# Optimization experiments

Measured on AMD Instinct MI355X. Metric: run time of the kernel, lower is better.

The kernel has to match this reference:

```python
import jax, jax.numpy as jnp
import numpy as np
import math

NUM_HEADS = 16
LOGIT_SCALE_MAX = math.log(1.0 / 0.01)  # log(100)
EPS = 1e-12


def _l2norm(x):
    # F.normalize(x, dim=-1): x / max(||x||_2, eps)
    n = jnp.sqrt(jnp.sum(x * x, axis=-1, keepdims=True))
    return x / jnp.maximum(n, EPS)


def setup_inputs() -> dict:
    key = jax.random.key(0)
    ks = jax.random.split(key, 6)
    N, B, C = 1024, 4, 1024
    scale = (C // NUM_HEADS) ** -0.5
    return {
        "query": jax.random.normal(ks[0], (N, B, C), jnp.float32),
        "key": jax.random.normal(ks[1], (N, B, C), jnp.float32),
        "value": jax.random.normal(ks[2], (N, B, C), jnp.float32),
        "in_proj_w": jax.random.normal(ks[3], (3 * C, C), jnp.float32) * scale,
        "in_proj_b": jnp.zeros((3 * C,), jnp.float32),
        "logit_scale": jnp.log(10.0) * jnp.ones((NUM_HEADS, 1, 1), jnp.float32),
        "out_w": jax.random.normal(ks[4], (C, C), jnp.float32) * scale,
        "out_b": jnp.zeros((C,), jnp.float32),
    }


def reference(query, key, value, in_proj_w, in_proj_b, logit_scale, out_w, out_b):
    N, B, C = query.shape
    H = NUM_HEADS
    hd = C // H
    # packed in-projection, split into q/k/v pieces
    w_q, w_k, w_v = jnp.split(in_proj_w, 3, axis=0)
    b_q, b_k, b_v = jnp.split(in_proj_b, 3, axis=0)
    q = query @ w_q.T + b_q          # (N, B, C)
    k = key @ w_k.T + b_k
    v = value @ w_v.T + b_v
    # (N, B, C) -> (B*H, N, hd)
    q = q.reshape(N, B * H, hd).swapaxes(0, 1)
    k = k.reshape(N, B * H, hd).swapaxes(0, 1)
    v = v.reshape(N, B * H, hd).swapaxes(0, 1)
    # cosine-similarity scores with learnable per-head logit scale
    attn = jnp.einsum('bqd,bkd->bqk', _l2norm(q), _l2norm(k))  # (B*H, N, N)
    ls = jnp.exp(jnp.minimum(logit_scale, LOGIT_SCALE_MAX))     # (H,1,1)
    attn = (attn.reshape(B, H, N, N) * ls).reshape(B * H, N, N)
    attn = jax.nn.softmax(attn, axis=-1)
    x = jnp.einsum('bqk,bkd->bqd', attn, v)                     # (B*H, N, hd)
    x = x.swapaxes(0, 1).reshape(N, B, C)
    return x @ out_w.T + out_b
```

## Files before the change

### kernel.cpp

```cpp
#include <hip/hip_runtime.h>


typedef _Float16 f16x8 __attribute__((ext_vector_type(8)));
typedef __fp16   h16x2 __attribute__((ext_vector_type(2)));
typedef float    f32x4 __attribute__((ext_vector_type(4)));

#define LOG2E 1.4426950408889634f
#define LOGMAX 4.6051702f

#define GLOAD16(g, l) \
    __builtin_amdgcn_global_load_lds((__attribute__((address_space(1))) void*)(g), \
                                     (__attribute__((address_space(3))) void*)(l), 16, 0, 0)

__device__ __forceinline__ unsigned short f2h(float x) {
    union { _Float16 h; unsigned short u; } cv;
    cv.h = (_Float16)x;
    return cv.u;
}

__global__ __launch_bounds__(256) void cvt_all(
    const float* __restrict__ q, const float* __restrict__ k,
    const float* __restrict__ v, const float* __restrict__ w,
    const float* __restrict__ ow,
    unsigned short* __restrict__ qbf, unsigned short* __restrict__ kbf,
    unsigned short* __restrict__ vbf, unsigned short* __restrict__ wbf,
    unsigned short* __restrict__ owbf)
{
    int b = blockIdx.x;
    const float* src; unsigned short* dst; int idx;
    if      (b < 4096)  { src = q;  dst = qbf;  idx = b; }
    else if (b < 8192)  { src = k;  dst = kbf;  idx = b - 4096; }
    else if (b < 12288) { src = v;  dst = vbf;  idx = b - 8192; }
    else if (b < 15360) { src = w;  dst = wbf;  idx = b - 12288; }
    else                { src = ow; dst = owbf; idx = b - 15360; }
    int i = idx * 256 + threadIdx.x;
    float4 val = ((const float4*)src)[i];
    ushort4 o;
    o.x = f2h(val.x); o.y = f2h(val.y); o.z = f2h(val.z); o.w = f2h(val.w);
    ((ushort4*)dst)[i] = o;
}

__global__ __launch_bounds__(256) void proj_gemm(
    const unsigned short* __restrict__ qbf, const unsigned short* __restrict__ kbf,
    const unsigned short* __restrict__ vbf, const unsigned short* __restrict__ wbf,
    const float* __restrict__ bias, const float* __restrict__ lsc,
    unsigned short* __restrict__ qn, unsigned short* __restrict__ kn,
    unsigned short* __restrict__ vT)
{
    __shared__ __align__(16) unsigned short AsmF[128 * 64];
    __shared__ __align__(16) unsigned short BsmF[128 * 64];
    int tid = threadIdx.x;
    int lane = tid & 63, wave = tid >> 6;
    int lr = lane & 15, lq = lane >> 4;
    int wr = wave >> 1, wc = wave & 1;

    int lin = blockIdx.x;
    int xcd = lin & 7, s = lin >> 3;
    int xt = s & 7, yy = (s >> 3) & 3, z = s >> 5;
    int m0 = (xcd * 4 + yy) * 128, n0 = xt * 128;

    const unsigned short* A = (z == 0) ? qbf : (z == 1) ? kbf : vbf;
    const unsigned short* W = wbf + (size_t)z * 1024 * 1024;

    int rl = lane >> 3;
    int cg = ((lane & 7) ^ rl) << 3;
    const unsigned short* gA = A + (size_t)(m0 + wave * 32 + rl) * 1024 + cg;
    const unsigned short* gB = W + (size_t)(n0 + wave * 32 + rl) * 1024 + cg;
    unsigned short* lA = &AsmF[wave * 32 * 64];
    unsigned short* lB = &BsmF[wave * 32 * 64];

    int swz = lr & 7;
    int c0 = (lq ^ swz) << 3;
    int c1 = ((lq ^ 4) ^ swz) << 3;

    f32x4 acc[4][4];
    for (int i = 0; i < 4; i++) for (int j = 0; j < 4; j++) acc[i][j] = (f32x4){0.f, 0.f, 0.f, 0.f};

    for (int ki = 0; ki < 16; ++ki) {
        for (int j = 0; j < 4; ++j) {
            GLOAD16(gA + ki * 64 + j * 8192, lA + j * 512);
            GLOAD16(gB + ki * 64 + j * 8192, lB + j * 512);
        }
        __syncthreads();
        for (int kc = 0; kc < 2; ++kc) {
            int co = kc ? c1 : c0;
            f16x8 af[4], bfr[4];
            for (int mi = 0; mi < 4; ++mi) af[mi]  = *(const f16x8*)&AsmF[(wr * 64 + mi * 16 + lr) * 64 + co];
            for (int ni = 0; ni < 4; ++ni) bfr[ni] = *(const f16x8*)&BsmF[(wc * 64 + ni * 16 + lr) * 64 + co];
            for (int mi = 0; mi < 4; ++mi)
                for (int ni = 0; ni < 4; ++ni)
                    acc[mi][ni] = __builtin_amdgcn_mfma_f32_16x16x32_f16(af[mi], bfr[ni], acc[mi][ni], 0, 0, 0);
        }
        __syncthreads();
    }

    int h = (n0 >> 6) + wc;
    float bv[4];
    for (int ni = 0; ni < 4; ++ni) bv[ni] = bias[z * 1024 + n0 + wc * 64 + ni * 16 + lr];
    for (int mi = 0; mi < 4; ++mi)
        for (int ni = 0; ni < 4; ++ni)
            for (int r = 0; r < 4; ++r) acc[mi][ni][r] += bv[ni];

    float lsfac = __expf(fminf(lsc[h], LOGMAX)) * LOG2E;

    for (int mi = 0; mi < 4; ++mi)
        for (int r = 0; r < 4; ++r) {
            int row = m0 + wr * 64 + mi * 16 + lq * 4 + r;
            int n = row >> 2, b = row & 3;
            int bh = b * 16 + h;
            if (z < 2) {
                float ss = 0.f;
                for (int ni = 0; ni < 4; ++ni) ss += acc[mi][ni][r] * acc[mi][ni][r];
                for (int off = 1; off < 16; off <<= 1) ss += __shfl_xor(ss, off);
                float scale = 1.0f / fmaxf(sqrtf(ss), 1e-12f);
                if (z == 0) scale *= lsfac;
                unsigned short* dst = (z == 0) ? qn : kn;
                for (int ni = 0; ni < 4; ++ni)
                    dst[(size_t)bh * 65536 + (size_t)n * 64 + ni * 16 + lr] = f2h(acc[mi][ni][r] * scale);
            } else {
                for (int ni = 0; ni < 4; ++ni)
                    vT[(size_t)bh * 65536 + (size_t)(ni * 16 + lr) * 1024 + n] = f2h(acc[mi][ni][r]);
            }
        }
}

__global__ __launch_bounds__(256) void flash_kernel(
    const unsigned short* __restrict__ qn, const unsigned short* __restrict__ kn,
    const unsigned short* __restrict__ vT, const float* __restrict__ lsc,
    unsigned short* __restrict__ xb)
{
    __shared__ __align__(16) unsigned short K_flat[2][64 * 64];
    __shared__ __align__(16) unsigned short V_flat[2][64 * 64];
    __shared__ __align__(16) unsigned short P_lds[4][2][16][72];
    int tid = threadIdx.x;
    int lane = tid & 63, wave = tid >> 6;
    int lr = lane & 15, lq = lane >> 4;

    int lin = blockIdx.x;
    int xcd = lin & 7, s = lin >> 3;
    int qt = s & 7, bh = xcd * 8 + (s >> 3);
    int q0 = qt * 128;

    float off = __expf(fminf(lsc[bh & 15], LOGMAX)) * LOG2E - 12.0f;
    f32x4 initv = (f32x4){-off, -off, -off, -off};

    f16x8 qf[2][2];
    for (int g = 0; g < 2; ++g)
        for (int kc = 0; kc < 2; ++kc)
            qf[g][kc] = *(const f16x8*)(qn + (size_t)bh * 65536 +
                          (size_t)(q0 + g * 64 + wave * 16 + lr) * 64 + kc * 32 + lq * 8);

    int rl = lane >> 3;
    int cg = ((lane & 7) ^ rl) << 3;
    const unsigned short* gK = kn + (size_t)bh * 65536 + (size_t)(wave * 16 + rl) * 64 + cg;
    const unsigned short* gV = vT + (size_t)bh * 65536 + (size_t)(wave * 16 + rl) * 1024 + cg;
    int swz = lr & 7;
    int c0 = (lq ^ swz) << 3;
    int c1 = ((lq ^ 4) ^ swz) << 3;

    f32x4 o[2][4];
    for (int g = 0; g < 2; ++g) for (int i = 0; i < 4; i++) o[g][i] = (f32x4){0.f, 0.f, 0.f, 0.f};
    float lsum[2] = {0.f, 0.f};

    {
        unsigned short* lK = &K_flat[0][wave * 16 * 64];
        unsigned short* lV = &V_flat[0][wave * 16 * 64];
        for (int j = 0; j < 2; ++j) {
            GLOAD16(gK + j * 512,  lK + j * 512);
            GLOAD16(gV + j * 8192, lV + j * 512);
        }
    }

    for (int kt = 0; kt < 16; ++kt) {
        int cur = kt & 1;
        __syncthreads();

        if (kt < 15) {
            unsigned short* lK = &K_flat[cur ^ 1][wave * 16 * 64];
            unsigned short* lV = &V_flat[cur ^ 1][wave * 16 * 64];
            for (int j = 0; j < 2; ++j) {
                GLOAD16(gK + (kt + 1) * 4096 + j * 512,  lK + j * 512);
                GLOAD16(gV + (kt + 1) * 64  + j * 8192,  lV + j * 512);
            }
        }

        f32x4 sc[2][4];
        __builtin_amdgcn_s_setprio(1);
        for (int ct = 0; ct < 4; ++ct) {
            for (int kc = 0; kc < 2; ++kc) {
                f16x8 kf = *(const f16x8*)&K_flat[cur][(ct * 16 + lr) * 64 + (kc ? c1 : c0)];
                for (int g = 0; g < 2; ++g)
                    sc[g][ct] = __builtin_amdgcn_mfma_f32_16x16x32_f16(
                        kf, qf[g][kc], kc == 0 ? initv : sc[g][ct], 0, 0, 0);
            }
        }
        __builtin_amdgcn_s_setprio(0);

        for (int g = 0; g < 2; ++g)
            for (int ct = 0; ct < 4; ++ct) {
                float p0 = __builtin_amdgcn_exp2f(sc[g][ct][0]);
                float p1 = __builtin_amdgcn_exp2f(sc[g][ct][1]);
                float p2 = __builtin_amdgcn_exp2f(sc[g][ct][2]);
                float p3 = __builtin_amdgcn_exp2f(sc[g][ct][3]);
                lsum[g] += (p0 + p1) + (p2 + p3);
                union { h16x2 h[2]; ushort4 u; } pw;
                pw.h[0] = __builtin_amdgcn_cvt_pkrtz(p0, p1);
                pw.h[1] = __builtin_amdgcn_cvt_pkrtz(p2, p3);
                *(ushort4*)&P_lds[wave][g][lr][ct * 16 + lq * 4] = pw.u;
            }

        f16x8 pf[2][2];
        for (int g = 0; g < 2; ++g)
            for (int kc = 0; kc < 2; ++kc)
                pf[g][kc] = *(const f16x8*)&P_lds[wave][g][lr][kc * 32 + lq * 8];
        __builtin_amdgcn_s_setprio(1);
        for (int nt = 0; nt < 4; ++nt)
            for (int kc = 0; kc < 2; ++kc) {
                f16x8 vf = *(const f16x8*)&V_flat[cur][(nt * 16 + lr) * 64 + (kc ? c1 : c0)];
                for (int g = 0; g < 2; ++g)
                    o[g][nt] = __builtin_amdgcn_mfma_f32_16x16x32_f16(vf, pf[g][kc], o[g][nt], 0, 0, 0);
            }
        __builtin_amdgcn_s_setprio(0);
    }

    int b = bh >> 4, h = bh & 15;
    for (int g = 0; g < 2; ++g) {
        float ls = lsum[g];
        ls += __shfl_xor(ls, 16);
        ls += __shfl_xor(ls, 32);
        float inv = 1.0f / ls;
        size_t m = (size_t)(q0 + g * 64 + wave * 16 + lr) * 4 + b;
        for (int nt = 0; nt < 4; ++nt) {
            ushort4 w;
            w.x = f2h(o[g][nt][0] * inv); w.y = f2h(o[g][nt][1] * inv);
            w.z = f2h(o[g][nt][2] * inv); w.w = f2h(o[g][nt][3] * inv);
            *(ushort4*)(xb + m * 1024 + h * 64 + nt * 16 + lq * 4) = w;
        }
    }
}

__global__ __launch_bounds__(256) void out_gemm(
    const unsigned short* __restrict__ xb, const unsigned short* __restrict__ owbf,
    const float* __restrict__ bias, float* __restrict__ outp)
{
    __shared__ __align__(16) unsigned short AsmF[128 * 64];
    __shared__ __align__(16) unsigned short BsmF[64 * 64];
    int tid = threadIdx.x;
    int lane = tid & 63, wave = tid >> 6;
    int lr = lane & 15, lq = lane >> 4;

    int lin = blockIdx.x;
    int xcd = lin & 7, s = lin >> 3;
    int xt = s & 15, yy = s >> 4;
    int m0 = (xcd * 4 + yy) * 128, n0 = xt * 64;

    int rl = lane >> 3;
    int cg = ((lane & 7) ^ rl) << 3;
    const unsigned short* gA = xb   + (size_t)(m0 + wave * 32 + rl) * 1024 + cg;
    const unsigned short* gB = owbf + (size_t)(n0 + wave * 16 + rl) * 1024 + cg;
    unsigned short* lA = &AsmF[wave * 32 * 64];
    unsigned short* lB = &BsmF[wave * 16 * 64];
    int swz = lr & 7;
    int c0 = (lq ^ swz) << 3;
    int c1 = ((lq ^ 4) ^ swz) << 3;

    f32x4 acc[2][4];
    for (int i = 0; i < 2; i++) for (int j = 0; j < 4; j++) acc[i][j] = (f32x4){0.f, 0.f, 0.f, 0.f};

    for (int ki = 0; ki < 16; ++ki) {
        for (int j = 0; j < 4; ++j)
            GLOAD16(gA + ki * 64 + j * 8192, lA + j * 512);
        for (int j = 0; j < 2; ++j)
            GLOAD16(gB + ki * 64 + j * 8192, lB + j * 512);
        __syncthreads();
        for (int kc = 0; kc < 2; ++kc) {
            int co = kc ? c1 : c0;
            f16x8 af[2], bfr[4];
            for (int mi = 0; mi < 2; ++mi) af[mi]  = *(const f16x8*)&AsmF[(wave * 32 + mi * 16 + lr) * 64 + co];
            for (int ni = 0; ni < 4; ++ni) bfr[ni] = *(const f16x8*)&BsmF[(ni * 16 + lr) * 64 + co];
            for (int mi = 0; mi < 2; ++mi)
                for (int ni = 0; ni < 4; ++ni)
                    acc[mi][ni] = __builtin_amdgcn_mfma_f32_16x16x32_f16(af[mi], bfr[ni], acc[mi][ni], 0, 0, 0);
        }
        __syncthreads();
    }
    for (int mi = 0; mi < 2; ++mi)
        for (int ni = 0; ni < 4; ++ni)
            for (int r = 0; r < 4; ++r) {
                int row = m0 + wave * 32 + mi * 16 + lq * 4 + r;
                int col = n0 + ni * 16 + lr;
                outp[(size_t)row * 1024 + col] = acc[mi][ni][r] + bias[col];
            }
}

extern "C" void kernel_launch(void* const* d_in, const int* in_sizes, int n_in,
                              void* d_out, int out_size, void* d_ws, size_t ws_size,
                              hipStream_t stream) {
    const float* query = (const float*)d_in[0];
    const float* key   = (const float*)d_in[1];
    const float* value = (const float*)d_in[2];
    const float* ipw   = (const float*)d_in[3];
    const float* ipb   = (const float*)d_in[4];
    const float* lsc   = (const float*)d_in[5];
    const float* ow    = (const float*)d_in[6];
    const float* ob    = (const float*)d_in[7];
    float* outp = (float*)d_out;

    char* ws = (char*)d_ws;
    unsigned short* qbf  = (unsigned short*)(ws);
    unsigned short* kbf  = (unsigned short*)(ws + 8388608);
    unsigned short* vbf  = (unsigned short*)(ws + 16777216);
    unsigned short* wbf  = (unsigned short*)(ws + 25165824);
    unsigned short* owbf = (unsigned short*)(ws + 31457280);
    unsigned short* qn   = (unsigned short*)(ws + 33554432);
    unsigned short* kn   = (unsigned short*)(ws + 41943040);
    unsigned short* vT   = (unsigned short*)(ws + 50331648);
    unsigned short* xbuf = (unsigned short*)(ws + 58720256);

    cvt_all<<<16384, 256, 0, stream>>>(query, key, value, ipw, ow,
                                       qbf, kbf, vbf, wbf, owbf);
    proj_gemm<<<768, 256, 0, stream>>>(qbf, kbf, vbf, wbf, ipb, lsc, qn, kn, vT);
    flash_kernel<<<512, 256, 0, stream>>>(qn, kn, vT, lsc, xbuf);
    out_gemm<<<512, 256, 0, stream>>>(xbuf, owbf, ob, outp);
}
```

Measured before the change: 203.8 us.

## Fuse fp32-to-fp16 conversion into GEMM loads with double-buffered LDS pipeline

Removes the separate conversion kernel and its fp16 workspace copies. proj_gemm and out_gemm now load fp32 inputs and weights into registers, convert them to fp16, and store them into double-buffered LDS, prefetching the next k-slice while MFMAs run. The goal is to avoid a full extra read/write pass over the activations and weights. In exchange the GEMMs read twice as many bytes per tile, use a smaller k-step of 32, and rely on register staging instead of direct global-to-LDS loads for the converted operands.

```diff
diff --git a/kernel.cpp b/kernel.cpp
--- a/kernel.cpp
+++ b/kernel.cpp
@@ -18,37 +18,22 @@
     return cv.u;
 }
 
-__global__ __launch_bounds__(256) void cvt_all(
-    const float* __restrict__ q, const float* __restrict__ k,
-    const float* __restrict__ v, const float* __restrict__ w,
-    const float* __restrict__ ow,
-    unsigned short* __restrict__ qbf, unsigned short* __restrict__ kbf,
-    unsigned short* __restrict__ vbf, unsigned short* __restrict__ wbf,
-    unsigned short* __restrict__ owbf)
-{
-    int b = blockIdx.x;
-    const float* src; unsigned short* dst; int idx;
-    if      (b < 4096)  { src = q;  dst = qbf;  idx = b; }
-    else if (b < 8192)  { src = k;  dst = kbf;  idx = b - 4096; }
-    else if (b < 12288) { src = v;  dst = vbf;  idx = b - 8192; }
-    else if (b < 15360) { src = w;  dst = wbf;  idx = b - 12288; }
-    else                { src = ow; dst = owbf; idx = b - 15360; }
-    int i = idx * 256 + threadIdx.x;
-    float4 val = ((const float4*)src)[i];
-    ushort4 o;
-    o.x = f2h(val.x); o.y = f2h(val.y); o.z = f2h(val.z); o.w = f2h(val.w);
-    ((ushort4*)dst)[i] = o;
+__device__ __forceinline__ f16x8 cvt8(float4 a, float4 b) {
+    f16x8 v;
+    v[0] = (_Float16)a.x; v[1] = (_Float16)a.y; v[2] = (_Float16)a.z; v[3] = (_Float16)a.w;
+    v[4] = (_Float16)b.x; v[5] = (_Float16)b.y; v[6] = (_Float16)b.z; v[7] = (_Float16)b.w;
+    return v;
 }
 
 __global__ __launch_bounds__(256) void proj_gemm(
-    const unsigned short* __restrict__ qbf, const unsigned short* __restrict__ kbf,
-    const unsigned short* __restrict__ vbf, const unsigned short* __restrict__ wbf,
+    const float* __restrict__ qsrc, const float* __restrict__ ksrc,
+    const float* __restrict__ vsrc, const float* __restrict__ wsrc,
     const float* __restrict__ bias, const float* __restrict__ lsc,
     unsigned short* __restrict__ qn, unsigned short* __restrict__ kn,
     unsigned short* __restrict__ vT)
 {
-    __shared__ __align__(16) unsigned short AsmF[128 * 64];
-    __shared__ __align__(16) unsigned short BsmF[128 * 64];
+    __shared__ __align__(16) unsigned short Asm[2][4096];
+    __shared__ __align__(16) unsigned short Bsm[2][4096];
     int tid = threadIdx.x;
     int lane = tid & 63, wave = tid >> 6;
     int lr = lane & 15, lq = lane >> 4;
@@ -59,39 +44,58 @@
     int xt = s & 7, yy = (s >> 3) & 3, z = s >> 5;
     int m0 = (xcd * 4 + yy) * 128, n0 = xt * 128;
 
-    const unsigned short* A = (z == 0) ? qbf : (z == 1) ? kbf : vbf;
-    const unsigned short* W = wbf + (size_t)z * 1024 * 1024;
-
-    int rl = lane >> 3;
-    int cg = ((lane & 7) ^ rl) << 3;
-    const unsigned short* gA = A + (size_t)(m0 + wave * 32 + rl) * 1024 + cg;
-    const unsigned short* gB = W + (size_t)(n0 + wave * 32 + rl) * 1024 + cg;
-    unsigned short* lA = &AsmF[wave * 32 * 64];
-    unsigned short* lB = &BsmF[wave * 32 * 64];
-
-    int swz = lr & 7;
-    int c0 = (lq ^ swz) << 3;
-    int c1 = ((lq ^ 4) ^ swz) << 3;
+    const float* A = (z == 0) ? qsrc : (z == 1) ? ksrc : vsrc;
+    const float* W = wsrc + (size_t)z * 1048576;
+
+    int r4 = lane >> 2, c4 = lane & 3;
+    int ssw = (r4 >> 1) & 3;
+    const float* gA = A + (size_t)(m0 + wave * 32 + r4) * 1024 + c4 * 8;
+    const float* gB = W + (size_t)(n0 + wave * 32 + r4) * 1024 + c4 * 8;
+    int wo = (wave * 32 + r4) * 32 + ((c4 ^ ssw) << 3);
+
+    int swz2 = (lr >> 1) & 3;
+    int co = (lq ^ swz2) << 3;
 
     f32x4 acc[4][4];
     for (int i = 0; i < 4; i++) for (int j = 0; j < 4; j++) acc[i][j] = (f32x4){0.f, 0.f, 0.f, 0.f};
 
-    for (int ki = 0; ki < 16; ++ki) {
-        for (int j = 0; j < 4; ++j) {
-            GLOAD16(gA + ki * 64 + j * 8192, lA + j * 512);
-            GLOAD16(gB + ki * 64 + j * 8192, lB + j * 512);
-        }
+    float4 ra[4], rb[4];
+    for (int j = 0; j < 2; ++j) {
+        ra[j*2]   = ((const float4*)(gA + j * 16384))[0];
+        ra[j*2+1] = ((const float4*)(gA + j * 16384))[1];
+        rb[j*2]   = ((const float4*)(gB + j * 16384))[0];
+        rb[j*2+1] = ((const float4*)(gB + j * 16384))[1];
+    }
+    for (int j = 0; j < 2; ++j) {
+        *(f16x8*)&Asm[0][wo + j*512] = cvt8(ra[j*2], ra[j*2+1]);
+        *(f16x8*)&Bsm[0][wo + j*512] = cvt8(rb[j*2], rb[j*2+1]);
+    }
+
+    for (int ks = 0; ks < 32; ++ks) {
+        int cur = ks & 1;
         __syncthreads();
-        for (int kc = 0; kc < 2; ++kc) {
-            int co = kc ? c1 : c0;
-            f16x8 af[4], bfr[4];
-            for (int mi = 0; mi < 4; ++mi) af[mi]  = *(const f16x8*)&AsmF[(wr * 64 + mi * 16 + lr) * 64 + co];
-            for (int ni = 0; ni < 4; ++ni) bfr[ni] = *(const f16x8*)&BsmF[(wc * 64 + ni * 16 + lr) * 64 + co];
-            for (int mi = 0; mi < 4; ++mi)
-                for (int ni = 0; ni < 4; ++ni)
-                    acc[mi][ni] = __builtin_amdgcn_mfma_f32_16x16x32_f16(af[mi], bfr[ni], acc[mi][ni], 0, 0, 0);
-        }
-        __syncthreads();
+        if (ks < 31) {
+            for (int j = 0; j < 2; ++j) {
+                ra[j*2]   = ((const float4*)(gA + (ks+1)*32 + j*16384))[0];
+                ra[j*2+1] = ((const float4*)(gA + (ks+1)*32 + j*16384))[1];
+                rb[j*2]   = ((const float4*)(gB + (ks+1)*32 + j*16384))[0];
+                rb[j*2+1] = ((const float4*)(gB + (ks+1)*32 + j*16384))[1];
+            }
+        }
+        f16x8 af[4], bfr[4];
+        for (int mi = 0; mi < 4; ++mi) af[mi]  = *(const f16x8*)&Asm[cur][(wr*64 + mi*16 + lr)*32 + co];
+        for (int ni = 0; ni < 4; ++ni) bfr[ni] = *(const f16x8*)&Bsm[cur][(wc*64 + ni*16 + lr)*32 + co];
+        __builtin_amdgcn_s_setprio(1);
+        for (int mi = 0; mi < 4; ++mi)
+            for (int ni = 0; ni < 4; ++ni)
+                acc[mi][ni] = __builtin_amdgcn_mfma_f32_16x16x32_f16(af[mi], bfr[ni], acc[mi][ni], 0, 0, 0);
+        __builtin_amdgcn_s_setprio(0);
+        if (ks < 31) {
+            for (int j = 0; j < 2; ++j) {
+                *(f16x8*)&Asm[cur^1][wo + j*512] = cvt8(ra[j*2], ra[j*2+1]);
+                *(f16x8*)&Bsm[cur^1][wo + j*512] = cvt8(rb[j*2], rb[j*2+1]);
+            }
+        }
     }
 
     int h = (n0 >> 6) + wc;
@@ -240,11 +244,11 @@
 }
 
 __global__ __launch_bounds__(256) void out_gemm(
-    const unsigned short* __restrict__ xb, const unsigned short* __restrict__ owbf,
+    const unsigned short* __restrict__ xb, const float* __restrict__ ow,
     const float* __restrict__ bias, float* __restrict__ outp)
 {
-    __shared__ __align__(16) unsigned short AsmF[128 * 64];
-    __shared__ __align__(16) unsigned short BsmF[64 * 64];
+    __shared__ __align__(16) unsigned short Asm[2][4096];
+    __shared__ __align__(16) unsigned short Bsm[2][2048];
     int tid = threadIdx.x;
     int lane = tid & 63, wave = tid >> 6;
     int lr = lane & 15, lq = lane >> 4;
@@ -254,36 +258,46 @@
     int xt = s & 15, yy = s >> 4;
     int m0 = (xcd * 4 + yy) * 128, n0 = xt * 64;
 
-    int rl = lane >> 3;
-    int cg = ((lane & 7) ^ rl) << 3;
-    const unsigned short* gA = xb   + (size_t)(m0 + wave * 32 + rl) * 1024 + cg;
-    const unsigned short* gB = owbf + (size_t)(n0 + wave * 16 + rl) * 1024 + cg;
-    unsigned short* lA = &AsmF[wave * 32 * 64];
-    unsigned short* lB = &BsmF[wave * 16 * 64];
-    int swz = lr & 7;
-    int c0 = (lq ^ swz) << 3;
-    int c1 = ((lq ^ 4) ^ swz) << 3;
+    int r4 = lane >> 2, c4 = lane & 3;
+    int ssw = (r4 >> 1) & 3;
+    const unsigned short* gA = xb + (size_t)(m0 + wave * 32 + r4) * 1024 + ((c4 ^ ssw) << 3);
+    const float* gB = ow + (size_t)(n0 + wave * 16 + r4) * 1024 + c4 * 8;
+    int wo_b = (wave * 16 + r4) * 32 + ((c4 ^ ssw) << 3);
+
+    int swz2 = (lr >> 1) & 3;
+    int co = (lq ^ swz2) << 3;
 
     f32x4 acc[2][4];
     for (int i = 0; i < 2; i++) for (int j = 0; j < 4; j++) acc[i][j] = (f32x4){0.f, 0.f, 0.f, 0.f};
 
-    for (int ki = 0; ki < 16; ++ki) {
-        for (int j = 0; j < 4; ++j)
-            GLOAD16(gA + ki * 64 + j * 8192, lA + j * 512);
-        for (int j = 0; j < 2; ++j)
-            GLOAD16(gB + ki * 64 + j * 8192, lB + j * 512);
+    float4 rb0, rb1;
+    for (int j = 0; j < 2; ++j)
+        GLOAD16(gA + j * 16384, &Asm[0][wave * 1024 + j * 512]);
+    rb0 = ((const float4*)gB)[0];
+    rb1 = ((const float4*)gB)[1];
+    *(f16x8*)&Bsm[0][wo_b] = cvt8(rb0, rb1);
+
+    for (int ks = 0; ks < 32; ++ks) {
+        int cur = ks & 1;
         __syncthreads();
-        for (int kc = 0; kc < 2; ++kc) {
-            int co = kc ? c1 : c0;
-            f16x8 af[2], bfr[4];
-            for (int mi = 0; mi < 2; ++mi) af[mi]  = *(const f16x8*)&AsmF[(wave * 32 + mi * 16 + lr) * 64 + co];
-            for (int ni = 0; ni < 4; ++ni) bfr[ni] = *(const f16x8*)&BsmF[(ni * 16 + lr) * 64 + co];
-            for (int mi = 0; mi < 2; ++mi)
-                for (int ni = 0; ni < 4; ++ni)
-                    acc[mi][ni] = __builtin_amdgcn_mfma_f32_16x16x32_f16(af[mi], bfr[ni], acc[mi][ni], 0, 0, 0);
-        }
-        __syncthreads();
-    }
+        if (ks < 31) {
+            for (int j = 0; j < 2; ++j)
+                GLOAD16(gA + (ks+1)*32 + j * 16384, &Asm[cur^1][wave * 1024 + j * 512]);
+            rb0 = ((const float4*)(gB + (ks+1)*32))[0];
+            rb1 = ((const float4*)(gB + (ks+1)*32))[1];
+        }
+        f16x8 af[2], bfr[4];
+        for (int mi = 0; mi < 2; ++mi) af[mi]  = *(const f16x8*)&Asm[cur][(wave*32 + mi*16 + lr)*32 + co];
+        for (int ni = 0; ni < 4; ++ni) bfr[ni] = *(const f16x8*)&Bsm[cur][(ni*16 + lr)*32 + co];
+        __builtin_amdgcn_s_setprio(1);
+        for (int mi = 0; mi < 2; ++mi)
+            for (int ni = 0; ni < 4; ++ni)
+                acc[mi][ni] = __builtin_amdgcn_mfma_f32_16x16x32_f16(af[mi], bfr[ni], acc[mi][ni], 0, 0, 0);
+        __builtin_amdgcn_s_setprio(0);
+        if (ks < 31)
+            *(f16x8*)&Bsm[cur^1][wo_b] = cvt8(rb0, rb1);
+    }
+
     for (int mi = 0; mi < 2; ++mi)
         for (int ni = 0; ni < 4; ++ni)
             for (int r = 0; r < 4; ++r) {
@@ -307,19 +321,12 @@
     float* outp = (float*)d_out;
 
     char* ws = (char*)d_ws;
-    unsigned short* qbf  = (unsigned short*)(ws);
-    unsigned short* kbf  = (unsigned short*)(ws + 8388608);
-    unsigned short* vbf  = (unsigned short*)(ws + 16777216);
-    unsigned short* wbf  = (unsigned short*)(ws + 25165824);
-    unsigned short* owbf = (unsigned short*)(ws + 31457280);
-    unsigned short* qn   = (unsigned short*)(ws + 33554432);
-    unsigned short* kn   = (unsigned short*)(ws + 41943040);
-    unsigned short* vT   = (unsigned short*)(ws + 50331648);
-    unsigned short* xbuf = (unsigned short*)(ws + 58720256);
-
-    cvt_all<<<16384, 256, 0, stream>>>(query, key, value, ipw, ow,
-                                       qbf, kbf, vbf, wbf, owbf);
-    proj_gemm<<<768, 256, 0, stream>>>(qbf, kbf, vbf, wbf, ipb, lsc, qn, kn, vT);
+    unsigned short* qn   = (unsigned short*)(ws);
+    unsigned short* kn   = (unsigned short*)(ws + 8388608);
+    unsigned short* vT   = (unsigned short*)(ws + 16777216);
+    unsigned short* xbuf = (unsigned short*)(ws + 25165824);
+
+    proj_gemm<<<768, 256, 0, stream>>>(query, key, value, ipw, ipb, lsc, qn, kn, vT);
     flash_kernel<<<512, 256, 0, stream>>>(qn, kn, vT, lsc, xbuf);
-    out_gemm<<<512, 256, 0, stream>>>(xbuf, owbf, ob, outp);
-}
+    out_gemm<<<512, 256, 0, stream>>>(xbuf, ow, ob, outp);
+}
```

After: 227.6 us. 1.12x slower.

## Double-buffer LDS tiles in projection GEMMs with K-step 32 prefetch

Applied to the files above, without the earlier changes.

Both the input-projection and output-projection GEMMs now use double-buffered shared memory tiles of K=32 instead of a single K=64 tile. The next tile's global-to-LDS load is issued before computing on the current one, and a single barrier per step replaces two. The intent is to hide global load latency behind MFMA work. The trade-off is twice as many loop iterations with less MFMA work per barrier, plus a changed swizzle for the narrower tile. There is also a possible race: the prefetch of step ks+1 is issued right after the barrier, with no explicit wait that guarantees the step ks loads have landed in LDS before they are read.

```diff
diff --git a/kernel.cpp b/kernel.cpp
--- a/kernel.cpp
+++ b/kernel.cpp
@@ -47,8 +47,8 @@
     unsigned short* __restrict__ qn, unsigned short* __restrict__ kn,
     unsigned short* __restrict__ vT)
 {
-    __shared__ __align__(16) unsigned short AsmF[128 * 64];
-    __shared__ __align__(16) unsigned short BsmF[128 * 64];
+    __shared__ __align__(16) unsigned short Asm[2][4096];
+    __shared__ __align__(16) unsigned short Bsm[2][4096];
     int tid = threadIdx.x;
     int lane = tid & 63, wave = tid >> 6;
     int lr = lane & 15, lq = lane >> 4;
@@ -60,38 +60,38 @@
     int m0 = (xcd * 4 + yy) * 128, n0 = xt * 128;
 
     const unsigned short* A = (z == 0) ? qbf : (z == 1) ? kbf : vbf;
-    const unsigned short* W = wbf + (size_t)z * 1024 * 1024;
-
-    int rl = lane >> 3;
-    int cg = ((lane & 7) ^ rl) << 3;
-    const unsigned short* gA = A + (size_t)(m0 + wave * 32 + rl) * 1024 + cg;
-    const unsigned short* gB = W + (size_t)(n0 + wave * 32 + rl) * 1024 + cg;
-    unsigned short* lA = &AsmF[wave * 32 * 64];
-    unsigned short* lB = &BsmF[wave * 32 * 64];
-
-    int swz = lr & 7;
-    int c0 = (lq ^ swz) << 3;
-    int c1 = ((lq ^ 4) ^ swz) << 3;
+    const unsigned short* W = wbf + (size_t)z * 1048576;
+
+    int r4 = lane >> 2, c4 = lane & 3;
+    int ssw = (r4 >> 1) & 3;
+    const unsigned short* gA = A + (size_t)(m0 + wave * 32 + r4) * 1024 + ((c4 ^ ssw) << 3);
+    const unsigned short* gB = W + (size_t)(n0 + wave * 32 + r4) * 1024 + ((c4 ^ ssw) << 3);
+
+    int co = (lq ^ ((lr >> 1) & 3)) << 3;
 
     f32x4 acc[4][4];
     for (int i = 0; i < 4; i++) for (int j = 0; j < 4; j++) acc[i][j] = (f32x4){0.f, 0.f, 0.f, 0.f};
 
-    for (int ki = 0; ki < 16; ++ki) {
-        for (int j = 0; j < 4; ++j) {
-            GLOAD16(gA + ki * 64 + j * 8192, lA + j * 512);
-            GLOAD16(gB + ki * 64 + j * 8192, lB + j * 512);
-        }
+    for (int j = 0; j < 2; ++j) {
+        GLOAD16(gA + j * 16384, &Asm[0][wave * 1024 + j * 512]);
+        GLOAD16(gB + j * 16384, &Bsm[0][wave * 1024 + j * 512]);
+    }
+
+    for (int ks = 0; ks < 32; ++ks) {
+        int cur = ks & 1;
         __syncthreads();
-        for (int kc = 0; kc < 2; ++kc) {
-            int co = kc ? c1 : c0;
-            f16x8 af[4], bfr[4];
-            for (int mi = 0; mi < 4; ++mi) af[mi]  = *(const f16x8*)&AsmF[(wr * 64 + mi * 16 + lr) * 64 + co];
-            for (int ni = 0; ni < 4; ++ni) bfr[ni] = *(const f16x8*)&BsmF[(wc * 64 + ni * 16 + lr) * 64 + co];
-            for (int mi = 0; mi < 4; ++mi)
-                for (int ni = 0; ni < 4; ++ni)
-                    acc[mi][ni] = __builtin_amdgcn_mfma_f32_16x16x32_f16(af[mi], bfr[ni], acc[mi][ni], 0, 0, 0);
-        }
-        __syncthreads();
+        if (ks < 31) {
+            for (int j = 0; j < 2; ++j) {
+                GLOAD16(gA + (ks + 1) * 32 + j * 16384, &Asm[cur ^ 1][wave * 1024 + j * 512]);
+                GLOAD16(gB + (ks + 1) * 32 + j * 16384, &Bsm[cur ^ 1][wave * 1024 + j * 512]);
+            }
+        }
+        f16x8 af[4], bfr[4];
+        for (int mi = 0; mi < 4; ++mi) af[mi]  = *(const f16x8*)&Asm[cur][(wr * 64 + mi * 16 + lr) * 32 + co];
+        for (int ni = 0; ni < 4; ++ni) bfr[ni] = *(const f16x8*)&Bsm[cur][(wc * 64 + ni * 16 + lr) * 32 + co];
+        for (int mi = 0; mi < 4; ++mi)
+            for (int ni = 0; ni < 4; ++ni)
+                acc[mi][ni] = __builtin_amdgcn_mfma_f32_16x16x32_f16(af[mi], bfr[ni], acc[mi][ni], 0, 0, 0);
     }
 
     int h = (n0 >> 6) + wc;
@@ -243,8 +243,8 @@
     const unsigned short* __restrict__ xb, const unsigned short* __restrict__ owbf,
     const float* __restrict__ bias, float* __restrict__ outp)
 {
-    __shared__ __align__(16) unsigned short AsmF[128 * 64];
-    __shared__ __align__(16) unsigned short BsmF[64 * 64];
+    __shared__ __align__(16) unsigned short Asm[2][4096];
+    __shared__ __align__(16) unsigned short Bsm[2][2048];
     int tid = threadIdx.x;
     int lane = tid & 63, wave = tid >> 6;
     int lr = lane & 15, lq = lane >> 4;
@@ -254,36 +254,36 @@
     int xt = s & 15, yy = s >> 4;
     int m0 = (xcd * 4 + yy) * 128, n0 = xt * 64;
 
-    int rl = lane >> 3;
-    int cg = ((lane & 7) ^ rl) << 3;
-    const unsigned short* gA = xb   + (size_t)(m0 + wave * 32 + rl) * 1024 + cg;
-    const unsigned short* gB = owbf + (size_t)(n0 + wave * 16 + rl) * 1024 + cg;
-    unsigned short* lA = &AsmF[wave * 32 * 64];
-    unsigned short* lB = &BsmF[wave * 16 * 64];
-    int swz = lr & 7;
-    int c0 = (lq ^ swz) << 3;
-    int c1 = ((lq ^ 4) ^ swz) << 3;
+    int r4 = lane >> 2, c4 = lane & 3;
+    int ssw = (r4 >> 1) & 3;
+    const unsigned short* gA = xb   + (size_t)(m0 + wave * 32 + r4) * 1024 + ((c4 ^ ssw) << 3);
+    const unsigned short* gB = owbf + (size_t)(n0 + wave * 16 + r4) * 1024 + ((c4 ^ ssw) << 3);
+
+    int co = (lq ^ ((lr >> 1) & 3)) << 3;
 
     f32x4 acc[2][4];
     for (int i = 0; i < 2; i++) for (int j = 0; j < 4; j++) acc[i][j] = (f32x4){0.f, 0.f, 0.f, 0.f};
 
-    for (int ki = 0; ki < 16; ++ki) {
-        for (int j = 0; j < 4; ++j)
-            GLOAD16(gA + ki * 64 + j * 8192, lA + j * 512);
-        for (int j = 0; j < 2; ++j)
-            GLOAD16(gB + ki * 64 + j * 8192, lB + j * 512);
+    for (int j = 0; j < 2; ++j)
+        GLOAD16(gA + j * 16384, &Asm[0][wave * 1024 + j * 512]);
+    GLOAD16(gB, &Bsm[0][wave * 512]);
+
+    for (int ks = 0; ks < 32; ++ks) {
+        int cur = ks & 1;
         __syncthreads();
-        for (int kc = 0; kc < 2; ++kc) {
-            int co = kc ? c1 : c0;
-            f16x8 af[2], bfr[4];
-            for (int mi = 0; mi < 2; ++mi) af[mi]  = *(const f16x8*)&AsmF[(wave * 32 + mi * 16 + lr) * 64 + co];
-            for (int ni = 0; ni < 4; ++ni) bfr[ni] = *(const f16x8*)&BsmF[(ni * 16 + lr) * 64 + co];
-            for (int mi = 0; mi < 2; ++mi)
-                for (int ni = 0; ni < 4; ++ni)
-                    acc[mi][ni] = __builtin_amdgcn_mfma_f32_16x16x32_f16(af[mi], bfr[ni], acc[mi][ni], 0, 0, 0);
-        }
-        __syncthreads();
-    }
+        if (ks < 31) {
+            for (int j = 0; j < 2; ++j)
+                GLOAD16(gA + (ks + 1) * 32 + j * 16384, &Asm[cur ^ 1][wave * 1024 + j * 512]);
+            GLOAD16(gB + (ks + 1) * 32, &Bsm[cur ^ 1][wave * 512]);
+        }
+        f16x8 af[2], bfr[4];
+        for (int mi = 0; mi < 2; ++mi) af[mi]  = *(const f16x8*)&Asm[cur][(wave * 32 + mi * 16 + lr) * 32 + co];
+        for (int ni = 0; ni < 4; ++ni) bfr[ni] = *(const f16x8*)&Bsm[cur][(ni * 16 + lr) * 32 + co];
+        for (int mi = 0; mi < 2; ++mi)
+            for (int ni = 0; ni < 4; ++ni)
+                acc[mi][ni] = __builtin_amdgcn_mfma_f32_16x16x32_f16(af[mi], bfr[ni], acc[mi][ni], 0, 0, 0);
+    }
+
     for (int mi = 0; mi < 2; ++mi)
         for (int ni = 0; ni < 4; ++ni)
             for (int r = 0; r < 4; ++r) {
```

Result: slower. 208.6 us (+2.4%).

## Double-buffer LDS tiles in projection and output GEMMs to overlap loads

Applied to the files above, without the earlier changes.

Both the input-projection GEMM and the output GEMM now keep two LDS buffers per operand. The next K-tile is prefetched with global_load_lds right after the barrier, while MFMAs run on the current tile, and the trailing barrier of each iteration is removed. The aim is to hide global-to-LDS latency behind compute. The cost is twice the shared memory per block (64 KB and 48 KB), which can reduce how many blocks fit on each CU.

```diff
diff --git a/kernel.cpp b/kernel.cpp
--- a/kernel.cpp
+++ b/kernel.cpp
@@ -47,8 +47,8 @@
     unsigned short* __restrict__ qn, unsigned short* __restrict__ kn,
     unsigned short* __restrict__ vT)
 {
-    __shared__ __align__(16) unsigned short AsmF[128 * 64];
-    __shared__ __align__(16) unsigned short BsmF[128 * 64];
+    __shared__ __align__(16) unsigned short Asm[2][128 * 64];
+    __shared__ __align__(16) unsigned short Bsm[2][128 * 64];
     int tid = threadIdx.x;
     int lane = tid & 63, wave = tid >> 6;
     int lr = lane & 15, lq = lane >> 4;
@@ -60,14 +60,12 @@
     int m0 = (xcd * 4 + yy) * 128, n0 = xt * 128;
 
     const unsigned short* A = (z == 0) ? qbf : (z == 1) ? kbf : vbf;
-    const unsigned short* W = wbf + (size_t)z * 1024 * 1024;
+    const unsigned short* W = wbf + (size_t)z * 1048576;
 
     int rl = lane >> 3;
     int cg = ((lane & 7) ^ rl) << 3;
     const unsigned short* gA = A + (size_t)(m0 + wave * 32 + rl) * 1024 + cg;
     const unsigned short* gB = W + (size_t)(n0 + wave * 32 + rl) * 1024 + cg;
-    unsigned short* lA = &AsmF[wave * 32 * 64];
-    unsigned short* lB = &BsmF[wave * 32 * 64];
 
     int swz = lr & 7;
     int c0 = (lq ^ swz) << 3;
@@ -76,22 +74,29 @@
     f32x4 acc[4][4];
     for (int i = 0; i < 4; i++) for (int j = 0; j < 4; j++) acc[i][j] = (f32x4){0.f, 0.f, 0.f, 0.f};
 
+    for (int j = 0; j < 4; ++j) {
+        GLOAD16(gA + j * 8192, &Asm[0][wave * 2048 + j * 512]);
+        GLOAD16(gB + j * 8192, &Bsm[0][wave * 2048 + j * 512]);
+    }
+
     for (int ki = 0; ki < 16; ++ki) {
-        for (int j = 0; j < 4; ++j) {
-            GLOAD16(gA + ki * 64 + j * 8192, lA + j * 512);
-            GLOAD16(gB + ki * 64 + j * 8192, lB + j * 512);
-        }
+        int cur = ki & 1;
         __syncthreads();
+        if (ki < 15) {
+            for (int j = 0; j < 4; ++j) {
+                GLOAD16(gA + (ki + 1) * 64 + j * 8192, &Asm[cur ^ 1][wave * 2048 + j * 512]);
+                GLOAD16(gB + (ki + 1) * 64 + j * 8192, &Bsm[cur ^ 1][wave * 2048 + j * 512]);
+            }
+        }
         for (int kc = 0; kc < 2; ++kc) {
             int co = kc ? c1 : c0;
             f16x8 af[4], bfr[4];
-            for (int mi = 0; mi < 4; ++mi) af[mi]  = *(const f16x8*)&AsmF[(wr * 64 + mi * 16 + lr) * 64 + co];
-            for (int ni = 0; ni < 4; ++ni) bfr[ni] = *(const f16x8*)&BsmF[(wc * 64 + ni * 16 + lr) * 64 + co];
+            for (int mi = 0; mi < 4; ++mi) af[mi]  = *(const f16x8*)&Asm[cur][(wr * 64 + mi * 16 + lr) * 64 + co];
+            for (int ni = 0; ni < 4; ++ni) bfr[ni] = *(const f16x8*)&Bsm[cur][(wc * 64 + ni * 16 + lr) * 64 + co];
             for (int mi = 0; mi < 4; ++mi)
                 for (int ni = 0; ni < 4; ++ni)
                     acc[mi][ni] = __builtin_amdgcn_mfma_f32_16x16x32_f16(af[mi], bfr[ni], acc[mi][ni], 0, 0, 0);
         }
-        __syncthreads();
     }
 
     int h = (n0 >> 6) + wc;
@@ -243,8 +248,8 @@
     const unsigned short* __restrict__ xb, const unsigned short* __restrict__ owbf,
     const float* __restrict__ bias, float* __restrict__ outp)
 {
-    __shared__ __align__(16) unsigned short AsmF[128 * 64];
-    __shared__ __align__(16) unsigned short BsmF[64 * 64];
+    __shared__ __align__(16) unsigned short Asm[2][128 * 64];
+    __shared__ __align__(16) unsigned short Bsm[2][64 * 64];
     int tid = threadIdx.x;
     int lane = tid & 63, wave = tid >> 6;
     int lr = lane & 15, lq = lane >> 4;
@@ -258,8 +263,6 @@
     int cg = ((lane & 7) ^ rl) << 3;
     const unsigned short* gA = xb   + (size_t)(m0 + wave * 32 + rl) * 1024 + cg;
     const unsigned short* gB = owbf + (size_t)(n0 + wave * 16 + rl) * 1024 + cg;
-    unsigned short* lA = &AsmF[wave * 32 * 64];
-    unsigned short* lB = &BsmF[wave * 16 * 64];
     int swz = lr & 7;
     int c0 = (lq ^ swz) << 3;
     int c1 = ((lq ^ 4) ^ swz) << 3;
@@ -267,22 +270,29 @@
     f32x4 acc[2][4];
     for (int i = 0; i < 2; i++) for (int j = 0; j < 4; j++) acc[i][j] = (f32x4){0.f, 0.f, 0.f, 0.f};
 
+    for (int j = 0; j < 4; ++j)
+        GLOAD16(gA + j * 8192, &Asm[0][wave * 2048 + j * 512]);
+    for (int j = 0; j < 2; ++j)
+        GLOAD16(gB + j * 8192, &Bsm[0][wave * 1024 + j * 512]);
+
     for (int ki = 0; ki < 16; ++ki) {
-        for (int j = 0; j < 4; ++j)
-            GLOAD16(gA + ki * 64 + j * 8192, lA + j * 512);
-        for (int j = 0; j < 2; ++j)
-            GLOAD16(gB + ki * 64 + j * 8192, lB + j * 512);
+        int cur = ki & 1;
         __syncthreads();
+        if (ki < 15) {
+            for (int j = 0; j < 4; ++j)
+                GLOAD16(gA + (ki + 1) * 64 + j * 8192, &Asm[cur ^ 1][wave * 2048 + j * 512]);
+            for (int j = 0; j < 2; ++j)
+                GLOAD16(gB + (ki + 1) * 64 + j * 8192, &Bsm[cur ^ 1][wave * 1024 + j * 512]);
+        }
         for (int kc = 0; kc < 2; ++kc) {
             int co = kc ? c1 : c0;
             f16x8 af[2], bfr[4];
-            for (int mi = 0; mi < 2; ++mi) af[mi]  = *(const f16x8*)&AsmF[(wave * 32 + mi * 16 + lr) * 64 + co];
-            for (int ni = 0; ni < 4; ++ni) bfr[ni] = *(const f16x8*)&BsmF[(ni * 16 + lr) * 64 + co];
+            for (int mi = 0; mi < 2; ++mi) af[mi]  = *(const f16x8*)&Asm[cur][(wave * 32 + mi * 16 + lr) * 64 + co];
+            for (int ni = 0; ni < 4; ++ni) bfr[ni] = *(const f16x8*)&Bsm[cur][(ni * 16 + lr) * 64 + co];
             for (int mi = 0; mi < 2; ++mi)
                 for (int ni = 0; ni < 4; ++ni)
                     acc[mi][ni] = __builtin_amdgcn_mfma_f32_16x16x32_f16(af[mi], bfr[ni], acc[mi][ni], 0, 0, 0);
         }
-        __syncthreads();
     }
     for (int mi = 0; mi < 2; ++mi)
         for (int ni = 0; ni < 4; ++ni)
```

New measurement: 214.2 us. 5.1% more time.
